# Kernel tuning notes

Hardware: AMD Instinct MI355X
Metric: run time of the kernel (lower is better)

## Reference

```python
import jax, jax.numpy as jnp
import numpy as np

B, D, N, OUT, H = 32768, 256, 4, 512, 4
DH = D // H


def _layer_norm(x, g, b, eps=1e-5):
    mu = jnp.mean(x, axis=-1, keepdims=True)
    var = jnp.mean(jnp.square(x - mu), axis=-1, keepdims=True)
    return (x - mu) * jax.lax.rsqrt(var + eps) * g + b


def setup_inputs() -> dict:
    key = jax.random.key(0)
    ks = jax.random.split(key, 32)
    s = lambda i, shape, scale=0.02: (jax.random.normal(ks[i], shape, jnp.float32) * scale)
    inp = {
        'w0': jax.random.normal(ks[0], (B, D), jnp.float32),
        'w1': jax.random.normal(ks[1], (B, D), jnp.float32),
        'w2': jax.random.normal(ks[2], (B, D), jnp.float32),
        'w3': jax.random.normal(ks[3], (B, D), jnp.float32),
        'regime': jax.random.uniform(ks[4], (B, 4), jnp.float32),
        'tf_weights': jnp.array([0.5, 1.0, 1.5, 2.0], jnp.float32),
        'in_proj_w': s(5, (3 * D, D)),
        'in_proj_b': s(6, (3 * D,)),
        'out_proj_w': s(7, (D, D)),
        'out_proj_b': s(8, (D,)),
        'ln1_g': jnp.ones((D,), jnp.float32),
        'ln1_b': jnp.zeros((D,), jnp.float32),
        'sg_w': s(9, (D, 4)),
        'sg_b': s(10, (D,)),
        'sb_w': s(11, (D, 4)),
        'sb_b': s(12, (D,)),
        'f1_w': s(13, (2 * OUT, D * N)),
        'f1_b': s(14, (2 * OUT,)),
        'f2_w': s(15, (OUT, 2 * OUT)),
        'f2_b': s(16, (OUT,)),
        'ln2_g': jnp.ones((OUT,), jnp.float32),
        'ln2_b': jnp.zeros((OUT,), jnp.float32),
        'a1_w': s(17, (128, D * N)),
        'a1_b': s(18, (128,)),
        'a2_w': s(19, (1, 128)),
        'a2_b': s(20, (1,)),
    }
    return inp


def _forward(w0, w1, w2, w3, regime, tf_weights, in_proj_w, in_proj_b,
             out_proj_w, out_proj_b, ln1_g, ln1_b, sg_w, sg_b, sb_w, sb_b,
             f1_w, f1_b, f2_w, f2_b, ln2_g, ln2_b, a1_w, a1_b, a2_w, a2_b):
    weights = jax.nn.softmax(tf_weights)  # [N]
    wav = jnp.stack([w0, w1, w2, w3], axis=1)  # [B, N, D]
    weighted = wav * weights[None, :, None]    # [B, N, D]
    query = weighted[:, 0, :]                  # [B, D]

    # MultiheadAttention: q_len=1, kv_len=N, H heads
    wq, wk, wv = in_proj_w[:D], in_proj_w[D:2 * D], in_proj_w[2 * D:]
    bq, bk, bv = in_proj_b[:D], in_proj_b[D:2 * D], in_proj_b[2 * D:]
    q = (query @ wq.T + bq).reshape(B, H, DH)              # [B, H, Dh]
    k = (weighted @ wk.T + bk).reshape(B, N, H, DH)        # [B, N, H, Dh]
    v = (weighted @ wv.T + bv).reshape(B, N, H, DH)
    scores = jnp.einsum('bhd,bnhd->bhn', q, k) / jnp.sqrt(jnp.float32(DH))
    attn = jax.nn.softmax(scores, axis=-1)                 # [B, H, N]
    ctx = jnp.einsum('bhn,bnhd->bhd', attn, v).reshape(B, D)
    attn_out = ctx @ out_proj_w.T + out_proj_b             # [B, D]

    entry = _layer_norm(query + attn_out, ln1_g, ln1_b)    # [B, D]
    gamma = regime @ sg_w.T + sg_b
    beta = regime @ sb_w.T + sb_b
    entry = entry * (1.0 + gamma) + beta                   # FiLM

    cat = jnp.concatenate([entry, weighted[:, 1, :], weighted[:, 2, :], weighted[:, 3, :]], axis=-1)  # [B, D*N]
    h = jax.nn.gelu(cat @ f1_w.T + f1_b, approximate=False)
    fused = _layer_norm(h @ f2_w.T + f2_b, ln2_g, ln2_b)   # [B, OUT]

    a = jax.nn.gelu(cat @ a1_w.T + a1_b, approximate=False)
    alignment = jax.nn.sigmoid(a @ a2_w.T + a2_b)          # [B, 1]
    return fused, alignment


def reference(w0, w1, w2, w3, regime, tf_weights, in_proj_w, in_proj_b,
              out_proj_w, out_proj_b, ln1_g, ln1_b, sg_w, sg_b, sb_w, sb_b,
              f1_w, f1_b, f2_w, f2_b, ln2_g, ln2_b, a1_w, a1_b, a2_w, a2_b):
    return _forward(w0, w1, w2, w3, regime, tf_weights, in_proj_w, in_proj_b,
                    out_proj_w, out_proj_b, ln1_g, ln1_b, sg_w, sg_b, sb_w, sb_b,
                    f1_w, f1_b, f2_w, f2_b, ln2_g, ln2_b, a1_w, a1_b, a2_w, a2_b)
```

## Files before the change

kernel.cpp:

```cpp
#include <hip/hip_runtime.h>
#include <math.h>

#define NB 32768

typedef unsigned short u16;
typedef __attribute__((ext_vector_type(4))) float f32x4;
typedef __attribute__((ext_vector_type(8))) short bf16x8;

__device__ __forceinline__ float bf2f(u16 u){ return __uint_as_float(((unsigned int)u)<<16); }
__device__ __forceinline__ u16 f2bf(float f){
    unsigned int x = __float_as_uint(f);
    x += 0x7fffu + ((x>>16)&1u);
    return (u16)(x>>16);
}
__device__ __forceinline__ float gelu_f(float x){
    float z = fabsf(x) * 0.70710678118654752f;
    float t = __builtin_amdgcn_rcpf(1.0f + 0.3275911f*z);
    float p = t*(0.254829592f + t*(-0.284496736f + t*(1.421413741f + t*(-1.453152027f + t*1.061405429f))));
    float e = __expf(-z*z);
    float erf_abs = 1.0f - p*e;
    float erfv = copysignf(erf_abs, x);
    return 0.5f*x*(1.0f + erfv);
}

__device__ __forceinline__ void gload16(const void* g, void* l){
    __builtin_amdgcn_global_load_lds(
        (const __attribute__((address_space(1))) unsigned int*)g,
        (__attribute__((address_space(3))) unsigned int*)l, 16, 0, 0);
}

__global__ __launch_bounds__(256) void prepconv_kernel(
    const float* __restrict__ w0, const float* __restrict__ w1,
    const float* __restrict__ w2, const float* __restrict__ w3,
    const float* __restrict__ tfw, u16* __restrict__ wcat,
    const float* __restrict__ ipw_s, u16* __restrict__ ipw_d,
    const float* __restrict__ op_s,  u16* __restrict__ op_d,
    const float* __restrict__ f1_s,  u16* __restrict__ f1_d,
    const float* __restrict__ f2_s,  u16* __restrict__ f2_d,
    const float* __restrict__ a1_s,  u16* __restrict__ a1_d)
{
    const int blk = blockIdx.x, tid = threadIdx.x;
    if (blk < 8192){
        float t0=tfw[0], t1=tfw[1], t2=tfw[2], t3=tfw[3];
        float m = fmaxf(fmaxf(t0,t1), fmaxf(t2,t3));
        float e0=expf(t0-m), e1=expf(t1-m), e2=expf(t2-m), e3=expf(t3-m);
        float inv = 1.0f/(e0+e1+e2+e3);
        float s0=e0*inv, s1=e1*inv, s2=e2*inv, s3=e3*inv;

        int idx = blk*256 + tid;
        int b  = idx >> 6;
        int d4 = (idx & 63) << 2;
        size_t src = (size_t)b*256 + d4;
        float4 a0 = *reinterpret_cast<const float4*>(w0 + src);
        float4 a1 = *reinterpret_cast<const float4*>(w1 + src);
        float4 a2 = *reinterpret_cast<const float4*>(w2 + src);
        float4 a3 = *reinterpret_cast<const float4*>(w3 + src);
        size_t dst = (size_t)b*1024 + d4;
        ushort4 o;
        o.x=f2bf(a0.x*s0); o.y=f2bf(a0.y*s0); o.z=f2bf(a0.z*s0); o.w=f2bf(a0.w*s0);
        *reinterpret_cast<ushort4*>(wcat + dst) = o;
        o.x=f2bf(a1.x*s1); o.y=f2bf(a1.y*s1); o.z=f2bf(a1.z*s1); o.w=f2bf(a1.w*s1);
        *reinterpret_cast<ushort4*>(wcat + dst + 256) = o;
        o.x=f2bf(a2.x*s2); o.y=f2bf(a2.y*s2); o.z=f2bf(a2.z*s2); o.w=f2bf(a2.w*s2);
        *reinterpret_cast<ushort4*>(wcat + dst + 512) = o;
        o.x=f2bf(a3.x*s3); o.y=f2bf(a3.y*s3); o.z=f2bf(a3.z*s3); o.w=f2bf(a3.w*s3);
        *reinterpret_cast<ushort4*>(wcat + dst + 768) = o;
    } else {
        int i = (blk - 8192)*256 + tid;
        const float* s; u16* d; int off;
        if      (i < 49152)  { s=ipw_s; d=ipw_d; off=i; }
        else if (i < 65536)  { s=op_s;  d=op_d;  off=i-49152; }
        else if (i < 327680) { s=f1_s;  d=f1_d;  off=i-65536; }
        else if (i < 458752) { s=f2_s;  d=f2_d;  off=i-327680; }
        else                 { s=a1_s;  d=a1_d;  off=i-458752; }
        float4 v = reinterpret_cast<const float4*>(s)[off];
        ushort4 o; o.x=f2bf(v.x); o.y=f2bf(v.y); o.z=f2bf(v.z); o.w=f2bf(v.w);
        reinterpret_cast<ushort4*>(d)[off] = o;
    }
}

template<int ACT>
__global__ __launch_bounds__(256) void mgemm_kernel(
    const u16* __restrict__ A, int lda,
    const u16* __restrict__ W, int ldw,
    const float* __restrict__ bias,
    u16* __restrict__ C, int ldc, int K,
    const float* __restrict__ a2w, const float* __restrict__ a2b, float* __restrict__ aln)
{
    __shared__ __align__(16) u16 sA[4096];
    __shared__ __align__(16) u16 sB[4096];

    const int tid  = threadIdx.x;
    const int lane = tid & 63;
    const int wid  = tid >> 6;
    const int wr   = wid >> 1, wc = wid & 1;
    const int row0 = blockIdx.x << 7, col0 = blockIdx.y << 7;

    const int e0 = tid << 3,          r0s = e0 >> 5, c0s = e0 & 31;
    const int e1 = (256 + tid) << 3,  r1s = e1 >> 5, c1s = e1 & 31;
    const u16* gA0 = A + (size_t)(row0 + r0s)*lda + c0s;
    const u16* gA1 = A + (size_t)(row0 + r1s)*lda + c1s;
    const u16* gB0 = W + (size_t)(col0 + r0s)*ldw + c0s;
    const u16* gB1 = W + (size_t)(col0 + r1s)*ldw + c1s;
    u16* lA0 = sA + (wid << 9);
    u16* lA1 = sA + 2048 + (wid << 9);
    u16* lB0 = sB + (wid << 9);
    u16* lB1 = sB + 2048 + (wid << 9);

    const int la  = lane & 15;
    const int lk  = (lane >> 4) << 3;
    const int hi4 = (lane >> 4) << 2;
    const u16* rA = sA + (((wr << 6) + la) << 5) + lk;
    const u16* rB = sB + (((wc << 6) + la) << 5) + lk;

    f32x4 acc[4][4];
    {
        f32x4 binit[4];
        #pragma unroll
        for (int n=0;n<4;n++){
            float4 b4 = *reinterpret_cast<const float4*>(bias + col0 + (wc<<6) + (n<<4) + hi4);
            binit[n] = (f32x4){b4.x, b4.y, b4.z, b4.w};
        }
        #pragma unroll
        for (int m=0;m<4;m++)
            #pragma unroll
            for (int n=0;n<4;n++) acc[m][n] = binit[n];
    }

    for (int k0 = 0; k0 < K; k0 += 32){
        gload16(gA0 + k0, lA0);
        gload16(gA1 + k0, lA1);
        gload16(gB0 + k0, lB0);
        gload16(gB1 + k0, lB1);
        __syncthreads();
        bf16x8 af[4], bf[4];
        #pragma unroll
        for (int m=0;m<4;m++) af[m] = *reinterpret_cast<const bf16x8*>(rA + (m << 9));
        #pragma unroll
        for (int n=0;n<4;n++) bf[n] = *reinterpret_cast<const bf16x8*>(rB + (n << 9));
        #pragma unroll
        for (int m=0;m<4;m++)
            #pragma unroll
            for (int n=0;n<4;n++)
                acc[m][n] = __builtin_amdgcn_mfma_f32_16x16x32_bf16(bf[n], af[m], acc[m][n], 0, 0, 0);
        __syncthreads();
    }

    if (ACT == 2){
        float w4[4][4];
        #pragma unroll
        for (int n=0;n<4;n++){
            float4 t4 = *reinterpret_cast<const float4*>(a2w + (wc<<6) + (n<<4) + hi4);
            w4[n][0]=t4.x; w4[n][1]=t4.y; w4[n][2]=t4.z; w4[n][3]=t4.w;
        }
        float* red = reinterpret_cast<float*>(sA);
        #pragma unroll
        for (int m=0;m<4;m++){
            float p = 0.f;
            #pragma unroll
            for (int n=0;n<4;n++){
                f32x4 v = acc[m][n];
                p += gelu_f(v[0])*w4[n][0] + gelu_f(v[1])*w4[n][1]
                   + gelu_f(v[2])*w4[n][2] + gelu_f(v[3])*w4[n][3];
            }
            red[(((wr<<6) + (m<<4) + la) << 3) + (wc<<2) + (lane>>4)] = p;
        }
        __syncthreads();
        if (tid < 128){
            float s = 0.f;
            #pragma unroll
            for (int k2=0;k2<8;k2++) s += red[(tid<<3)+k2];
            aln[row0 + tid] = 1.0f/(1.0f + __expf(-(s + a2b[0])));
        }
        return;
    }

    #pragma unroll
    for (int m=0;m<4;m++){
        const int grow = row0 + (wr << 6) + (m << 4) + la;
        u16* crow = C + (size_t)grow*ldc + col0 + (wc << 6) + hi4;
        #pragma unroll
        for (int n=0;n<4;n++){
            f32x4 v = acc[m][n];
            float x0=v[0], x1=v[1], x2=v[2], x3=v[3];
            if (ACT == 1){ x0=gelu_f(x0); x1=gelu_f(x1); x2=gelu_f(x2); x3=gelu_f(x3); }
            ushort4 o; o.x=f2bf(x0); o.y=f2bf(x1); o.z=f2bf(x2); o.w=f2bf(x3);
            *reinterpret_cast<ushort4*>(crow + (n << 4)) = o;
        }
    }
}

template<int ACT>
__global__ __launch_bounds__(512) void gemm256p_kernel(
    const u16* __restrict__ A, int lda,
    const u16* __restrict__ W, int ldw,
    const float* __restrict__ bias,
    u16* __restrict__ C, int ldc, int K)
{
    __shared__ __align__(16) u16 sT[65536];

    const int tid  = threadIdx.x;
    const int lane = tid & 63;
    const int wid  = tid >> 6;
    const int wr   = wid >> 2;
    const int wc   = wid & 3;
    const int row0 = blockIdx.x << 8, col0 = blockIdx.y << 8;

    const int la = lane & 15;
    const int hi = lane >> 4;

    f32x4 acc[8][4];
    {
        f32x4 binit[4];
        #pragma unroll
        for (int n=0;n<4;n++){
            float4 b4 = *reinterpret_cast<const float4*>(bias + col0 + (wc<<6) + (n<<4) + (hi<<2));
            binit[n] = (f32x4){b4.x, b4.y, b4.z, b4.w};
        }
        #pragma unroll
        for (int m=0;m<8;m++)
            #pragma unroll
            for (int n=0;n<4;n++) acc[m][n] = binit[n];
    }

    const int rs = (wid << 4) + (lane >> 3);
    const int cs = ((lane & 7) ^ ((lane >> 3) & 7)) << 3;
    const u16* gA0 = A + (size_t)(row0 + rs)*lda + cs;
    const u16* gA1 = gA0 + (size_t)128*lda;
    const u16* gB0 = W + (size_t)(col0 + rs)*ldw + cs;
    const u16* gB1 = gB0 + (size_t)128*ldw;
    const int ldsw = (wid << 4) * 64;

    const int cph0 = (hi ^ (la & 7)) << 3;
    const u16* rAbase = sT + ((wr << 7) + la)*64;
    const u16* rBbase = sT + 16384 + ((wc << 6) + la)*64;

    const int NT = K >> 6;

    gload16(gB0, sT + 16384 + ldsw);          gload16(gB0 + 8*(size_t)ldw, sT + 16384 + ldsw + 512);
    gload16(gB1, sT + 24576 + ldsw);          gload16(gB1 + 8*(size_t)ldw, sT + 24576 + ldsw + 512);
    gload16(gA0, sT + ldsw);                  gload16(gA0 + 8*(size_t)lda, sT + ldsw + 512);
    gload16(gA1, sT + 8192 + ldsw);           gload16(gA1 + 8*(size_t)lda, sT + 8192 + ldsw + 512);

#define STG(GP, LD, DOFF) \
        gload16(GP + kb, sT + bn + (DOFF) + ldsw); \
        gload16(GP + kb + 8*(size_t)(LD), sT + bn + (DOFF) + ldsw + 512);

#define DSRA(MH, CO) { \
        const u16* rA_ = rAbase + b + ((MH) << 12) + (CO); \
        af[0] = *reinterpret_cast<const bf16x8*>(rA_); \
        af[1] = *reinterpret_cast<const bf16x8*>(rA_ + 1024); \
        af[2] = *reinterpret_cast<const bf16x8*>(rA_ + 2048); \
        af[3] = *reinterpret_cast<const bf16x8*>(rA_ + 3072); }

#define DSRB(CO) { \
        const u16* rB_ = rBbase + b + (CO); \
        bf[0] = *reinterpret_cast<const bf16x8*>(rB_); \
        bf[1] = *reinterpret_cast<const bf16x8*>(rB_ + 1024); \
        bf[2] = *reinterpret_cast<const bf16x8*>(rB_ + 2048); \
        bf[3] = *reinterpret_cast<const bf16x8*>(rB_ + 3072); }

#define MFMA16(MB) { \
        _Pragma("unroll") \
        for (int m=0;m<4;m++){ \
            _Pragma("unroll") \
            for (int n=0;n<4;n++) \
                acc[(MB)+m][n] = __builtin_amdgcn_mfma_f32_16x16x32_bf16(bf[n], af[m], acc[(MB)+m][n], 0,0,0); \
        } }

    for (int t = 0; t < NT; ++t){
        const int b  = (t & 1) << 15;
        const int bn = b ^ 32768;
        const bool stg = (t + 1 < NT);
        const int kb = (t + 1) << 6;
        bf16x8 af[4], bf[4];
        const int co0 = cph0;
        const int co1 = cph0 ^ 32;

        asm volatile("s_waitcnt vmcnt(0)" ::: "memory");
        __builtin_amdgcn_s_barrier();
        __builtin_amdgcn_sched_barrier(0);
        DSRB(co0)
        DSRA(0, co0)
        if (stg){ STG(gB0, ldw, 16384) }
        MFMA16(0)
        DSRA(1, co0)
        if (stg){ STG(gB1, ldw, 24576) }
        __builtin_amdgcn_sched_barrier(0);
        __builtin_amdgcn_s_barrier();
        __builtin_amdgcn_sched_barrier(0);
        MFMA16(4)
        DSRB(co1)
        DSRA(0, co1)
        if (stg){ STG(gA0, lda, 0) }
        __builtin_amdgcn_sched_barrier(0);
        __builtin_amdgcn_s_barrier();
        __builtin_amdgcn_sched_barrier(0);
        MFMA16(0)
        DSRA(1, co1)
        if (stg){ STG(gA1, lda, 8192) }
        __builtin_amdgcn_sched_barrier(0);
        __builtin_amdgcn_s_barrier();
        __builtin_amdgcn_sched_barrier(0);
        MFMA16(4)
    }
#undef STG
#undef DSRA
#undef DSRB
#undef MFMA16

    #pragma unroll
    for (int m=0;m<8;m++){
        const int grow = row0 + (wr << 7) + (m << 4) + la;
        u16* crow = C + (size_t)grow*ldc + col0 + (wc << 6) + (hi << 2);
        #pragma unroll
        for (int n=0;n<4;n++){
            f32x4 v = acc[m][n];
            float x0=v[0], x1=v[1], x2=v[2], x3=v[3];
            if (ACT == 1){ x0=gelu_f(x0); x1=gelu_f(x1); x2=gelu_f(x2); x3=gelu_f(x3); }
            ushort4 o; o.x=f2bf(x0); o.y=f2bf(x1); o.z=f2bf(x2); o.w=f2bf(x3);
            *reinterpret_cast<ushort4*>(crow + (n << 4)) = o;
        }
    }
}

__global__ __launch_bounds__(256) void attnop_kernel(
    const u16* __restrict__ q, const u16* __restrict__ kv,
    u16* __restrict__ wcat,
    const u16* __restrict__ opw, const float* __restrict__ opb,
    const float* __restrict__ regime,
    const float* __restrict__ sgw, const float* __restrict__ sgb,
    const float* __restrict__ sbw, const float* __restrict__ sbb,
    const float* __restrict__ g1, const float* __restrict__ b1)
{
    __shared__ __align__(16) u16 sKV[32768];
    __shared__ __align__(16) u16 sQC[16*264];
    __shared__ float sAT[256];

    const int t  = threadIdx.x;
    const int b0 = blockIdx.x << 4;

    {
        const int row = t >> 4, u = t & 15;
        const u16* qsrc = q + (size_t)(b0 + row)*256 + (u << 4);
        *reinterpret_cast<bf16x8*>(sQC + row*264 + (u<<4))     = *reinterpret_cast<const bf16x8*>(qsrc);
        *reinterpret_cast<bf16x8*>(sQC + row*264 + (u<<4) + 8) = *reinterpret_cast<const bf16x8*>(qsrc + 8);
        const u16* kvsrc = kv + (size_t)b0*2048;
        #pragma unroll
        for (int j=0;j<16;j++){
            const int off = (t<<3) + j*2048;
            *reinterpret_cast<bf16x8*>(sKV + off) = *reinterpret_cast<const bf16x8*>(kvsrc + off);
        }
    }
    __syncthreads();

    {
        const int s = t >> 4, h = (t >> 2) & 3, n = t & 3;
        float sc = 0.f;
        const u16* qp = sQC + s*264 + h*64;
        const u16* kp = sKV + s*2048 + n*512 + h*64;
        #pragma unroll
        for (int dh=0; dh<64; ++dh) sc += bf2f(qp[dh]) * bf2f(kp[dh]);
        sc *= 0.125f;
        float m = fmaxf(sc, __shfl_xor(sc, 1)); m = fmaxf(m, __shfl_xor(m, 2));
        float e = __expf(sc - m);
        float sum = e + __shfl_xor(e, 1); sum += __shfl_xor(sum, 2);
        sAT[t] = e / sum;
    }
    __syncthreads();

    {
        const int s = t >> 4, u = t & 15;
        #pragma unroll
        for (int j=0;j<16;j++){
            const int d = (u << 4) + j;
            const int h = d >> 6;
            const float* a = sAT + s*16 + (h<<2);
            const u16* vp = sKV + s*2048 + 256 + d;
            float c = a[0]*bf2f(vp[0]) + a[1]*bf2f(vp[512]) + a[2]*bf2f(vp[1024]) + a[3]*bf2f(vp[1536]);
            sQC[s*264 + d] = f2bf(c);
        }
    }
    __syncthreads();

    float* sAO = reinterpret_cast<float*>(sKV);
    {
        const int lane = t & 63, wid = t >> 6;
        const int la = lane & 15, hi = lane >> 4;
        f32x4 acc[4];
        #pragma unroll
        for (int n=0;n<4;n++){
            float4 b4 = *reinterpret_cast<const float4*>(opb + (wid<<6) + (n<<4) + (hi<<2));
            acc[n] = (f32x4){b4.x, b4.y, b4.z, b4.w};
        }
        #pragma unroll
        for (int ks=0; ks<8; ++ks){
            bf16x8 af = *reinterpret_cast<const bf16x8*>(sQC + la*264 + (ks<<5) + (hi<<3));
            #pragma unroll
            for (int n=0;n<4;n++){
                bf16x8 wf = *reinterpret_cast<const bf16x8*>(
                    opw + (size_t)((wid<<6) + (n<<4) + la)*256 + (ks<<5) + (hi<<3));
                acc[n] = __builtin_amdgcn_mfma_f32_16x16x32_bf16(wf, af, acc[n], 0, 0, 0);
            }
        }
        #pragma unroll
        for (int n=0;n<4;n++){
            float4 st = {acc[n][0], acc[n][1], acc[n][2], acc[n][3]};
            *reinterpret_cast<float4*>(sAO + la*264 + (wid<<6) + (n<<4) + (hi<<2)) = st;
        }
    }
    __syncthreads();

    {
        const int s = t >> 4, u = t & 15;
        u16* qrow = wcat + (size_t)(b0 + s)*1024;
        float xv[16], sum = 0.f, sq = 0.f;
        #pragma unroll
        for (int j=0;j<16;j++){
            const int d = u + (j << 4);
            float x = sAO[s*264 + d] + bf2f(qrow[d]);
            xv[j] = x; sum += x; sq += x*x;
        }
        #pragma unroll
        for (int o=1;o<16;o<<=1){ sum += __shfl_xor(sum, o); sq += __shfl_xor(sq, o); }
        float mu   = sum * (1.0f/256.0f);
        float var  = sq  * (1.0f/256.0f) - mu*mu;
        float rstd = rsqrtf(var + 1e-5f);
        const float r0 = regime[(b0+s)*4+0], r1 = regime[(b0+s)*4+1];
        const float r2 = regime[(b0+s)*4+2], r3 = regime[(b0+s)*4+3];
        #pragma unroll
        for (int j=0;j<16;j++){
            const int d = u + (j << 4);
            float gam = r0*sgw[d*4+0] + r1*sgw[d*4+1] + r2*sgw[d*4+2] + r3*sgw[d*4+3] + sgb[d];
            float bet = r0*sbw[d*4+0] + r1*sbw[d*4+1] + r2*sbw[d*4+2] + r3*sbw[d*4+3] + sbb[d];
            float e = ((xv[j]-mu)*rstd*g1[d] + b1[d])*(1.0f+gam) + bet;
            qrow[d] = f2bf(e);
        }
    }
}

__global__ __launch_bounds__(256) void ln2_kernel(
    const u16* __restrict__ t1, const float* __restrict__ g, const float* __restrict__ bt,
    float* __restrict__ out)
{
    const int b = blockIdx.x, t = threadIdx.x;
    float x0 = bf2f(t1[(size_t)b*512 + t]);
    float x1 = bf2f(t1[(size_t)b*512 + 256 + t]);
    float s = x0+x1, q = x0*x0 + x1*x1;
    #pragma unroll
    for (int o=32;o;o>>=1){ s += __shfl_xor(s,o); q += __shfl_xor(q,o); }
    __shared__ float rs[4], rq[4];
    if ((t&63)==0){ rs[t>>6]=s; rq[t>>6]=q; }
    __syncthreads();
    s = rs[0]+rs[1]+rs[2]+rs[3];
    q = rq[0]+rq[1]+rq[2]+rq[3];
    float mu  = s*(1.0f/512.0f);
    float var = q*(1.0f/512.0f) - mu*mu;
    float rstd = rsqrtf(var + 1e-5f);
    out[(size_t)b*512 + t]       = (x0-mu)*rstd*g[t]     + bt[t];
    out[(size_t)b*512 + 256 + t] = (x1-mu)*rstd*g[256+t] + bt[256+t];
}

extern "C" void kernel_launch(void* const* d_in, const int* in_sizes, int n_in,
                              void* d_out, int out_size, void* d_ws, size_t ws_size,
                              hipStream_t stream) {
    const float* w0   = (const float*)d_in[0];
    const float* w1   = (const float*)d_in[1];
    const float* w2   = (const float*)d_in[2];
    const float* w3   = (const float*)d_in[3];
    const float* regime = (const float*)d_in[4];
    const float* tfw  = (const float*)d_in[5];
    const float* in_proj_w = (const float*)d_in[6];
    const float* in_proj_b = (const float*)d_in[7];
    const float* out_proj_w = (const float*)d_in[8];
    const float* out_proj_b = (const float*)d_in[9];
    const float* ln1_g = (const float*)d_in[10];
    const float* ln1_b = (const float*)d_in[11];
    const float* sg_w = (const float*)d_in[12];
    const float* sg_b = (const float*)d_in[13];
    const float* sb_w = (const float*)d_in[14];
    const float* sb_b = (const float*)d_in[15];
    const float* f1_w = (const float*)d_in[16];
    const float* f1_b = (const float*)d_in[17];
    const float* f2_w = (const float*)d_in[18];
    const float* f2_b = (const float*)d_in[19];
    const float* ln2_g = (const float*)d_in[20];
    const float* ln2_b = (const float*)d_in[21];
    const float* a1_w = (const float*)d_in[22];
    const float* a1_b = (const float*)d_in[23];
    const float* a2_w = (const float*)d_in[24];
    const float* a2_b = (const float*)d_in[25];

    char* ws = (char*)d_ws;
    u16* wcat  = (u16*)(ws);
    u16* qbuf  = (u16*)(ws + 67108864ull);
    u16* kvbuf = (u16*)(ws + 83886080ull);
    u16* hbuf  = kvbuf;
    u16* t1buf = (u16*)(ws + 150994944ull);
    u16* wb    = (u16*)(ws + 218103808ull);
    u16* ipw = wb;
    u16* opw = wb + 196608;
    u16* f1w = wb + 262144;
    u16* f2w = wb + 1310720;
    u16* a1w = wb + 1835008;

    float* out_fused = (float*)d_out;
    float* out_align = (float*)d_out + (size_t)NB*512;

    prepconv_kernel<<<10112, 256, 0, stream>>>(w0,w1,w2,w3,tfw,wcat,
        in_proj_w,ipw, out_proj_w,opw, f1_w,f1w, f2_w,f2w, a1_w,a1w);
    mgemm_kernel<0><<<dim3(256, 2), 256, 0, stream>>>(wcat, 1024, ipw, 256, in_proj_b, qbuf, 256, 256, nullptr, nullptr, nullptr);
    gemm256p_kernel<0><<<dim3(512, 2), 512, 0, stream>>>(wcat, 256, ipw+65536, 256, in_proj_b+256, kvbuf, 512, 256);
    attnop_kernel<<<2048, 256, 0, stream>>>(qbuf, kvbuf, wcat, opw, out_proj_b,
        regime, sg_w, sg_b, sb_w, sb_b, ln1_g, ln1_b);
    gemm256p_kernel<1><<<dim3(128, 4), 512, 0, stream>>>(wcat, 1024, f1w, 1024, f1_b, hbuf, 1024, 1024);
    gemm256p_kernel<0><<<dim3(128, 2), 512, 0, stream>>>(hbuf, 1024, f2w, 1024, f2_b, t1buf, 512, 1024);
    ln2_kernel<<<NB, 256, 0, stream>>>(t1buf, ln2_g, ln2_b, out_fused);
    mgemm_kernel<2><<<dim3(256, 1), 256, 0, stream>>>(wcat, 1024, a1w, 1024, a1_b, qbuf, 128, 1024, a2_w, a2_b, out_align);
}
```

Baseline: 342.6 us.

## Fuse Q projection into attention kernel and F2 GEMM with LayerNorm

The Q projection is now computed inside the attention kernel with MFMA on the query rows already staged in shared memory. This removes a separate GEMM launch and the write and read of a Q buffer. The F2 GEMM and the second LayerNorm are merged into one kernel with 128-row tiles that span all 512 output columns, so the row statistics are taken from shared memory and the bf16 intermediate never goes to global memory. In exchange, the fused F2 kernel launches only 256 blocks with a large shared-memory footprint, which may lower occupancy and leave compute units underused.

```diff
diff --git a/kernel.cpp b/kernel.cpp
--- a/kernel.cpp
+++ b/kernel.cpp
@@ -325,8 +325,9 @@
 }
 
 __global__ __launch_bounds__(256) void attnop_kernel(
-    const u16* __restrict__ q, const u16* __restrict__ kv,
+    const u16* __restrict__ kv,
     u16* __restrict__ wcat,
+    const u16* __restrict__ ipw, const float* __restrict__ ipb,
     const u16* __restrict__ opw, const float* __restrict__ opb,
     const float* __restrict__ regime,
     const float* __restrict__ sgw, const float* __restrict__ sgb,
@@ -342,7 +343,7 @@
 
     {
         const int row = t >> 4, u = t & 15;
-        const u16* qsrc = q + (size_t)(b0 + row)*256 + (u << 4);
+        const u16* qsrc = wcat + (size_t)(b0 + row)*1024 + (u << 4);
         *reinterpret_cast<bf16x8*>(sQC + row*264 + (u<<4))     = *reinterpret_cast<const bf16x8*>(qsrc);
         *reinterpret_cast<bf16x8*>(sQC + row*264 + (u<<4) + 8) = *reinterpret_cast<const bf16x8*>(qsrc + 8);
         const u16* kvsrc = kv + (size_t)b0*2048;
@@ -350,6 +351,38 @@
         for (int j=0;j<16;j++){
             const int off = (t<<3) + j*2048;
             *reinterpret_cast<bf16x8*>(sKV + off) = *reinterpret_cast<const bf16x8*>(kvsrc + off);
+        }
+    }
+    __syncthreads();
+
+    const int lane = t & 63, wid = t >> 6;
+    const int la = lane & 15, hi = lane >> 4;
+    f32x4 qacc[4];
+    {
+        #pragma unroll
+        for (int n=0;n<4;n++){
+            float4 b4 = *reinterpret_cast<const float4*>(ipb + (wid<<6) + (n<<4) + (hi<<2));
+            qacc[n] = (f32x4){b4.x, b4.y, b4.z, b4.w};
+        }
+        #pragma unroll
+        for (int kk=0; kk<8; ++kk){
+            bf16x8 af = *reinterpret_cast<const bf16x8*>(sQC + la*264 + (kk<<5) + (hi<<3));
+            #pragma unroll
+            for (int n=0;n<4;n++){
+                bf16x8 wf = *reinterpret_cast<const bf16x8*>(
+                    ipw + (size_t)((wid<<6) + (n<<4) + la)*256 + (kk<<5) + (hi<<3));
+                qacc[n] = __builtin_amdgcn_mfma_f32_16x16x32_bf16(wf, af, qacc[n], 0, 0, 0);
+            }
+        }
+    }
+    __syncthreads();
+    {
+        #pragma unroll
+        for (int n=0;n<4;n++){
+            ushort4 o;
+            o.x = f2bf(qacc[n][0]); o.y = f2bf(qacc[n][1]);
+            o.z = f2bf(qacc[n][2]); o.w = f2bf(qacc[n][3]);
+            *reinterpret_cast<ushort4*>(sQC + la*264 + (wid<<6) + (n<<4) + (hi<<2)) = o;
         }
     }
     __syncthreads();
@@ -385,8 +418,6 @@
 
     float* sAO = reinterpret_cast<float*>(sKV);
     {
-        const int lane = t & 63, wid = t >> 6;
-        const int la = lane & 15, hi = lane >> 4;
         f32x4 acc[4];
         #pragma unroll
         for (int n=0;n<4;n++){
@@ -439,26 +470,133 @@
     }
 }
 
-__global__ __launch_bounds__(256) void ln2_kernel(
-    const u16* __restrict__ t1, const float* __restrict__ g, const float* __restrict__ bt,
+__global__ __launch_bounds__(512) void f2ln_kernel(
+    const u16* __restrict__ A,
+    const u16* __restrict__ W,
+    const float* __restrict__ bias,
+    const float* __restrict__ g, const float* __restrict__ bt,
     float* __restrict__ out)
 {
-    const int b = blockIdx.x, t = threadIdx.x;
-    float x0 = bf2f(t1[(size_t)b*512 + t]);
-    float x1 = bf2f(t1[(size_t)b*512 + 256 + t]);
-    float s = x0+x1, q = x0*x0 + x1*x1;
+    __shared__ __align__(16) u16 sT[66560];
+
+    const int tid  = threadIdx.x;
+    const int lane = tid & 63;
+    const int wid  = tid >> 6;
+    const int wr   = wid >> 2;
+    const int wc   = wid & 3;
+    const int row0 = blockIdx.x << 7;
+
+    const int la = lane & 15;
+    const int hi = lane >> 4;
+
+    f32x4 acc[4][8];
+    {
+        #pragma unroll
+        for (int n=0;n<8;n++){
+            float4 b4 = *reinterpret_cast<const float4*>(bias + (wc<<7) + (n<<4) + (hi<<2));
+            f32x4 bi = (f32x4){b4.x, b4.y, b4.z, b4.w};
+            #pragma unroll
+            for (int m=0;m<4;m++) acc[m][n] = bi;
+        }
+    }
+
+    const int rsA = (wid << 4) + (lane >> 2);
+    const int rsB = (wid << 6) + (lane >> 2);
+    const int swA = ((lane & 3) ^ ((rsA >> 1) & 3)) << 3;
+    const int swB = ((lane & 3) ^ ((rsB >> 1) & 3)) << 3;
+    const u16* pA = A + (size_t)(row0 + rsA)*1024 + swA;
+    const u16* pB = W + (size_t)rsB*1024 + swB;
+
+    const int cph0 = (hi ^ ((la >> 1) & 3)) << 3;
+
+    const int NT = 32;
+
+    gload16(pA, sT + (wid<<9));
     #pragma unroll
-    for (int o=32;o;o>>=1){ s += __shfl_xor(s,o); q += __shfl_xor(q,o); }
-    __shared__ float rs[4], rq[4];
-    if ((t&63)==0){ rs[t>>6]=s; rq[t>>6]=q; }
+    for (int j=0;j<4;j++) gload16(pB + (size_t)(j<<4)*1024, sT + 4096 + (wid<<11) + (j<<9));
+
+    for (int t = 0; t < NT; ++t){
+        const int b  = (t & 1) ? 20480 : 0;
+        const int bn = b ? 0 : 20480;
+        const int kb = (t + 1) << 5;
+
+        asm volatile("s_waitcnt vmcnt(0)" ::: "memory");
+        __builtin_amdgcn_s_barrier();
+        __builtin_amdgcn_sched_barrier(0);
+
+        if (t + 1 < NT){
+            gload16(pA + kb, sT + bn + (wid<<9));
+            #pragma unroll
+            for (int j=0;j<4;j++) gload16(pB + (size_t)(j<<4)*1024 + kb, sT + bn + 4096 + (wid<<11) + (j<<9));
+        }
+
+        bf16x8 af[4], bf[8];
+        #pragma unroll
+        for (int m=0;m<4;m++){
+            const int r = (wr<<6) + (m<<4) + la;
+            af[m] = *reinterpret_cast<const bf16x8*>(sT + b + (r<<5) + cph0);
+        }
+        #pragma unroll
+        for (int n=0;n<8;n++){
+            const int r = (wc<<7) + (n<<4) + la;
+            bf[n] = *reinterpret_cast<const bf16x8*>(sT + b + 4096 + (r<<5) + cph0);
+        }
+        #pragma unroll
+        for (int m=0;m<4;m++)
+            #pragma unroll
+            for (int n=0;n<8;n++)
+                acc[m][n] = __builtin_amdgcn_mfma_f32_16x16x32_bf16(bf[n], af[m], acc[m][n], 0, 0, 0);
+    }
+
+    __builtin_amdgcn_s_barrier();
+    #pragma unroll
+    for (int m=0;m<4;m++){
+        const int r = (wr<<6) + (m<<4) + la;
+        u16* rowp = sT + r*520 + (wc<<7) + (hi<<2);
+        #pragma unroll
+        for (int n=0;n<8;n++){
+            ushort4 o;
+            o.x = f2bf(acc[m][n][0]); o.y = f2bf(acc[m][n][1]);
+            o.z = f2bf(acc[m][n][2]); o.w = f2bf(acc[m][n][3]);
+            *reinterpret_cast<ushort4*>(rowp + (n<<4)) = o;
+        }
+    }
     __syncthreads();
-    s = rs[0]+rs[1]+rs[2]+rs[3];
-    q = rq[0]+rq[1]+rq[2]+rq[3];
-    float mu  = s*(1.0f/512.0f);
-    float var = q*(1.0f/512.0f) - mu*mu;
-    float rstd = rsqrtf(var + 1e-5f);
-    out[(size_t)b*512 + t]       = (x0-mu)*rstd*g[t]     + bt[t];
-    out[(size_t)b*512 + 256 + t] = (x1-mu)*rstd*g[256+t] + bt[256+t];
+
+    {
+        const int r  = tid >> 2;
+        const int q4 = tid & 3;
+        const u16* rowp = sT + r*520 + (q4<<7);
+        float sum = 0.f, sq = 0.f;
+        #pragma unroll
+        for (int i=0;i<16;i++){
+            bf16x8 v = *reinterpret_cast<const bf16x8*>(rowp + (i<<3));
+            #pragma unroll
+            for (int k=0;k<8;k++){ float x = bf2f((u16)v[k]); sum += x; sq += x*x; }
+        }
+        sum += __shfl_xor(sum, 1); sq += __shfl_xor(sq, 1);
+        sum += __shfl_xor(sum, 2); sq += __shfl_xor(sq, 2);
+        float mu   = sum * (1.0f/512.0f);
+        float var  = sq  * (1.0f/512.0f) - mu*mu;
+        float rstd = rsqrtf(var + 1e-5f);
+        float* orow = out + (size_t)(row0 + r)*512 + (q4<<7);
+        #pragma unroll
+        for (int i=0;i<16;i++){
+            bf16x8 v = *reinterpret_cast<const bf16x8*>(rowp + (i<<3));
+            const int c0 = (q4<<7) + (i<<3);
+            float4 o0, o1;
+            o0.x = (bf2f((u16)v[0])-mu)*rstd*g[c0+0] + bt[c0+0];
+            o0.y = (bf2f((u16)v[1])-mu)*rstd*g[c0+1] + bt[c0+1];
+            o0.z = (bf2f((u16)v[2])-mu)*rstd*g[c0+2] + bt[c0+2];
+            o0.w = (bf2f((u16)v[3])-mu)*rstd*g[c0+3] + bt[c0+3];
+            o1.x = (bf2f((u16)v[4])-mu)*rstd*g[c0+4] + bt[c0+4];
+            o1.y = (bf2f((u16)v[5])-mu)*rstd*g[c0+5] + bt[c0+5];
+            o1.z = (bf2f((u16)v[6])-mu)*rstd*g[c0+6] + bt[c0+6];
+            o1.w = (bf2f((u16)v[7])-mu)*rstd*g[c0+7] + bt[c0+7];
+            *reinterpret_cast<float4*>(orow + (i<<3))     = o0;
+            *reinterpret_cast<float4*>(orow + (i<<3) + 4) = o1;
+        }
+    }
 }
 
 extern "C" void kernel_launch(void* const* d_in, const int* in_sizes, int n_in,
@@ -493,10 +631,9 @@
 
     char* ws = (char*)d_ws;
     u16* wcat  = (u16*)(ws);
-    u16* qbuf  = (u16*)(ws + 67108864ull);
     u16* kvbuf = (u16*)(ws + 83886080ull);
     u16* hbuf  = kvbuf;
-    u16* t1buf = (u16*)(ws + 150994944ull);
+    u16* dummy = (u16*)(ws + 67108864ull);
     u16* wb    = (u16*)(ws + 218103808ull);
     u16* ipw = wb;
     u16* opw = wb + 196608;
@@ -509,12 +646,10 @@
 
     prepconv_kernel<<<10112, 256, 0, stream>>>(w0,w1,w2,w3,tfw,wcat,
         in_proj_w,ipw, out_proj_w,opw, f1_w,f1w, f2_w,f2w, a1_w,a1w);
-    mgemm_kernel<0><<<dim3(256, 2), 256, 0, stream>>>(wcat, 1024, ipw, 256, in_proj_b, qbuf, 256, 256, nullptr, nullptr, nullptr);
     gemm256p_kernel<0><<<dim3(512, 2), 512, 0, stream>>>(wcat, 256, ipw+65536, 256, in_proj_b+256, kvbuf, 512, 256);
-    attnop_kernel<<<2048, 256, 0, stream>>>(qbuf, kvbuf, wcat, opw, out_proj_b,
+    attnop_kernel<<<2048, 256, 0, stream>>>(kvbuf, wcat, ipw, in_proj_b, opw, out_proj_b,
         regime, sg_w, sg_b, sb_w, sb_b, ln1_g, ln1_b);
     gemm256p_kernel<1><<<dim3(128, 4), 512, 0, stream>>>(wcat, 1024, f1w, 1024, f1_b, hbuf, 1024, 1024);
-    gemm256p_kernel<0><<<dim3(128, 2), 512, 0, stream>>>(hbuf, 1024, f2w, 1024, f2_b, t1buf, 512, 1024);
-    ln2_kernel<<<NB, 256, 0, stream>>>(t1buf, ln2_g, ln2_b, out_fused);
-    mgemm_kernel<2><<<dim3(256, 1), 256, 0, stream>>>(wcat, 1024, a1w, 1024, a1_b, qbuf, 128, 1024, a2_w, a2_b, out_align);
-}
+    f2ln_kernel<<<256, 512, 0, stream>>>(hbuf, f2w, f2_b, ln2_g, ln2_b, out_fused);
+    mgemm_kernel<2><<<dim3(256, 1), 256, 0, stream>>>(wcat, 1024, a1w, 1024, a1_b, dummy, 128, 1024, a2_w, a2_b, out_align);
+}
```

After: 367.1 us. 7.1% more time.
